# Kernel tuning notes

Measured on AMD Instinct MI355X. Metric: run time of the kernel, lower is better.

## Reference

```python
import jax, jax.numpy as jnp
import numpy as np
import math

MODEL_DIM = 1024
NUM_HEADS = 16
ATTN_DIM = MODEL_DIM // NUM_HEADS  # 64
ROWS, COLS, AXES = 32, 32, 2
PAIRS = ATTN_DIM // (AXES * 2)     # 16
BATCH = 4
TOKENS = ROWS * COLS               # 1024


def setup_inputs() -> dict:
    key = jax.random.key(0)
    ks = jax.random.split(key, 8)
    s = 1.0 / math.sqrt(MODEL_DIM)
    return {
        "x": jax.random.normal(ks[0], (BATCH, TOKENS, MODEL_DIM), jnp.float32),
        "cos": jax.random.uniform(ks[1], (ROWS, COLS, AXES, PAIRS), jnp.float32),
        "sin": jax.random.uniform(ks[2], (ROWS, COLS, AXES, PAIRS), jnp.float32),
        "Wq": jax.random.normal(ks[3], (MODEL_DIM, MODEL_DIM), jnp.float32) * s,
        "Wk": jax.random.normal(ks[4], (MODEL_DIM, MODEL_DIM), jnp.float32) * s,
        "Wv": jax.random.normal(ks[5], (MODEL_DIM, MODEL_DIM), jnp.float32) * s,
        "Wo": jax.random.normal(ks[6], (MODEL_DIM, MODEL_DIM), jnp.float32) * s,
        "bo": jax.random.normal(ks[7], (MODEL_DIM,), jnp.float32) * 0.01,
    }


def _apply_rope(W, cos, sin):
    # W: (b, h, tokens, attn_dim) -> (b, h, rows, cols, axes, pairs, 2)
    b, h, n, d = W.shape
    rows, cols, axes, pairs = cos.shape
    Wp = W.reshape(b, h, rows, cols, axes, pairs, 2)
    c = cos[None, None]
    s = sin[None, None]
    w0, w1 = Wp[..., 0], Wp[..., 1]
    out = jnp.stack([c * w0 - s * w1, s * w0 + c * w1], axis=-1)
    return out.reshape(b, h, n, d)


def reference(x, cos, sin, Wq, Wk, Wv, Wo, bo):
    b, n, _ = x.shape
    # torch Linear: y = x @ W.T
    Q = (x @ Wq.T).reshape(b, n, NUM_HEADS, ATTN_DIM).transpose(0, 2, 1, 3)
    K = (x @ Wk.T).reshape(b, n, NUM_HEADS, ATTN_DIM).transpose(0, 2, 1, 3)
    V = (x @ Wv.T).reshape(b, n, NUM_HEADS, ATTN_DIM).transpose(0, 2, 1, 3)
    Q = _apply_rope(Q, cos, sin)
    K = _apply_rope(K, cos, sin)
    scores = jnp.einsum("bhqd,bhkd->bhqk", Q, K) / math.sqrt(ATTN_DIM)
    attn = jax.nn.softmax(scores, axis=-1)
    o = jnp.einsum("bhqk,bhkd->bhqd", attn, V)
    o = o.transpose(0, 2, 1, 3).reshape(b, n, MODEL_DIM)
    return o @ Wo.T + bo
```

## Files before the change

kernel.cpp:

```cpp
#include <hip/hip_runtime.h>
#include <hip/hip_bf16.h>

typedef __bf16 bf16;
typedef __bf16 bf16x4 __attribute__((ext_vector_type(4)));
typedef __bf16 bf16x8 __attribute__((ext_vector_type(8)));
typedef float  f32x4  __attribute__((ext_vector_type(4)));
typedef unsigned int u32x2 __attribute__((ext_vector_type(2)));

#define MFMA16(a, b, c) __builtin_amdgcn_mfma_f32_16x16x32_bf16((a), (b), (c), 0, 0, 0)

#define GLOBAL_AS(p) ((const __attribute__((address_space(1))) void*)(p))
#define LDS_AS(p)    ((__attribute__((address_space(3))) void*)(p))

#define BATCH 4
#define TOK   1024
#define DIM   1024
#define HEADS 16
#define HD    64
#define MTOT  (BATCH * TOK)
#define MELEM (1024u * 1024u)

__global__ __launch_bounds__(256) void k_prep(
    const float* __restrict__ X,
    const float* __restrict__ W0, const float* __restrict__ W1,
    const float* __restrict__ W2, const float* __restrict__ W3,
    bf16* __restrict__ xh, bf16* __restrict__ wsp)
{
    const int bid = blockIdx.x;
    if (bid < 2048) {
        size_t i0 = ((size_t)bid * 256 + threadIdx.x) * 8;
        f32x4 a = *(const f32x4*)(X + i0);
        f32x4 b = *(const f32x4*)(X + i0 + 4);
        bf16x8 h;
        #pragma unroll
        for (int j = 0; j < 4; j++) { h[j] = (bf16)a[j]; h[4 + j] = (bf16)b[j]; }
        *(bf16x8*)(xh + i0) = h;
    } else {
        const int b2 = bid - 2048;
        const int widx = b2 >> 9;
        const int inner = b2 & 511;
        const float* W = (widx == 0) ? W0 : (widx == 1) ? W1 : (widx == 2) ? W2 : W3;
        size_t i0 = ((size_t)inner * 256 + threadIdx.x) * 8;
        f32x4 a = *(const f32x4*)(W + i0);
        f32x4 b = *(const f32x4*)(W + i0 + 4);
        bf16x8 h, l;
        #pragma unroll
        for (int j = 0; j < 4; j++) {
            bf16 g0 = (bf16)a[j]; h[j] = g0;     l[j] = (bf16)(a[j] - (float)g0);
            bf16 g1 = (bf16)b[j]; h[4 + j] = g1; l[4 + j] = (bf16)(b[j] - (float)g1);
        }
        *(bf16x8*)(wsp + (size_t)widx * MELEM + i0) = h;
        if (widx == 3)
            *(bf16x8*)(wsp + 4 * (size_t)MELEM + i0) = l;
    }
}

__global__ __launch_bounds__(512) void k_gemmQKV(
    const bf16* __restrict__ Ag, const bf16* __restrict__ wsp,
    const float* __restrict__ cosT, const float* __restrict__ sinT,
    bf16* __restrict__ q_o, bf16* __restrict__ k_o, bf16* __restrict__ v_o)
{
    __shared__ bf16 lds[24576];
    bf16* A0 = lds;
    bf16* A1 = lds + 4096;
    bf16* B0 = lds + 8192;
    bf16* B1 = lds + 16384;

    const int fid = blockIdx.x;
    const int swz = (fid & 7) * 48 + (fid >> 3);
    const int nt = swz % 12;
    const int mt = swz / 12;

    const int t = threadIdx.x;
    const int lane = t & 63;
    const int w = t >> 6;
    const int wr = w >> 2, wc = w & 3;
    const int l15 = lane & 15;
    const int grp = lane >> 4;

    f32x4 acc[4][4];
    #pragma unroll
    for (int m = 0; m < 4; m++)
        #pragma unroll
        for (int n = 0; n < 4; n++)
            #pragma unroll
            for (int r = 0; r < 4; r++) acc[m][n][r] = 0.f;

    const int srow = lane >> 2;
    const int schk8 = ((lane & 3) ^ ((lane >> 3) & 3)) * 8;
    const bf16* asrc = Ag  + (size_t)(mt * 128 + srow) * DIM + schk8;
    const bf16* bsrc = wsp + (size_t)(nt * 256 + srow) * DIM + schk8;

    auto stage = [&](int k, bf16* ab, bf16* bb) {
        const int k0 = k * 32;
        __builtin_amdgcn_global_load_lds(
            GLOBAL_AS(asrc + (size_t)w * 16 * DIM + k0),
            LDS_AS(ab + w * 512), 16, 0, 0);
        #pragma unroll
        for (int jj = 0; jj < 2; ++jj) {
            int j = w * 2 + jj;
            __builtin_amdgcn_global_load_lds(
                GLOBAL_AS(bsrc + (size_t)j * 16 * DIM + k0),
                LDS_AS(bb + j * 512), 16, 0, 0);
        }
    };

    auto compute = [&](const bf16* ab, const bf16* bb) {
        bf16x8 fb[4];
        #pragma unroll
        for (int n = 0; n < 4; n++) {
            int rb = wc * 64 + n * 16 + l15;
            fb[n] = *(const bf16x8*)&bb[rb * 32 + ((grp ^ ((rb >> 1) & 3)) << 3)];
        }
        __builtin_amdgcn_s_setprio(1);
        #pragma unroll
        for (int m = 0; m < 4; m++) {
            int r = wr * 64 + m * 16 + l15;
            bf16x8 fa = *(const bf16x8*)&ab[r * 32 + ((grp ^ ((r >> 1) & 3)) << 3)];
            #pragma unroll
            for (int n = 0; n < 4; n++)
                acc[m][n] = MFMA16(fa, fb[n], acc[m][n]);
        }
        __builtin_amdgcn_s_setprio(0);
    };

    stage(0, A0, B0);
    #pragma unroll 1
    for (int kk = 0; kk < 16; kk++) {
        __syncthreads();
        stage(2 * kk + 1, A1, B1);
        compute(A0, B0);
        __syncthreads();
        if (kk < 15) stage(2 * kk + 2, A0, B0);
        compute(A1, B1);
    }

    const int mode = nt >> 2;
    const int h = (nt & 3) * 4 + wc;
    if (mode == 2) {
        #pragma unroll
        for (int m = 0; m < 4; m++) {
            const int grow0 = mt * 128 + wr * 64 + m * 16 + grp * 4;
            const int b = grow0 >> 10, ntok0 = grow0 & (TOK - 1);
            #pragma unroll
            for (int n = 0; n < 4; n++) {
                const int d = n * 16 + l15;
                bf16x4 pk;
                #pragma unroll
                for (int r = 0; r < 4; r++) pk[r] = (bf16)acc[m][n][r];
                *(bf16x4*)&v_o[((size_t)((b * HEADS + h) * HD + d)) * TOK + ntok0] = pk;
            }
        }
    } else {
        __syncthreads();
        float* cosL = (float*)lds;
        float* sinL = (float*)(lds + 8192);
        const int tb = (mt & 7) * 128;
        *(f32x4*)(cosL + t * 8)     = *(const f32x4*)(cosT + (size_t)tb * 32 + t * 8);
        *(f32x4*)(cosL + t * 8 + 4) = *(const f32x4*)(cosT + (size_t)tb * 32 + t * 8 + 4);
        *(f32x4*)(sinL + t * 8)     = *(const f32x4*)(sinT + (size_t)tb * 32 + t * 8);
        *(f32x4*)(sinL + t * 8 + 4) = *(const f32x4*)(sinT + (size_t)tb * 32 + t * 8 + 4);
        __syncthreads();

        bf16* dst = (mode == 0) ? q_o : k_o;
        const float sc = (mode == 0) ? 0.18033688f : 1.0f;
        #pragma unroll
        for (int m = 0; m < 4; m++) {
            const int grow0 = mt * 128 + wr * 64 + m * 16 + grp * 4;
            const int b = grow0 >> 10, ntok0 = grow0 & (TOK - 1);
            const int loc0 = wr * 64 + m * 16 + grp * 4;
            #pragma unroll
            for (int n = 0; n < 4; n++) {
                const int d = n * 16 + l15;
                const int idp = (d >> 5) * 16 + ((d >> 1) & 15);
                const bool ev = (d & 1) == 0;
                #pragma unroll
                for (int r = 0; r < 4; r++) {
                    float v = acc[m][n][r];
                    float pr = __shfl_xor(v, 1, 64);
                    float c = cosL[(loc0 + r) * 32 + idp];
                    float s = sinL[(loc0 + r) * 32 + idp];
                    float res = (ev ? (c * v - s * pr) : (s * pr + c * v)) * sc;
                    dst[((size_t)(b * HEADS + h) * TOK + ntok0 + r) * HD + d] = (bf16)res;
                }
            }
        }
    }
}

__global__ __launch_bounds__(256) void k_gemmO(
    const bf16* __restrict__ Ag, const bf16* __restrict__ wsp,
    const float* __restrict__ bo, float* __restrict__ f_o)
{
    __shared__ bf16 Alin[64 * 64];
    __shared__ bf16 Bhlin[128 * 64];
    __shared__ bf16 Bllin[128 * 64];

    const bf16* Bh_g = wsp + 3 * (size_t)MELEM;
    const bf16* Bl_g = wsp + 4 * (size_t)MELEM;

    const int fid = blockIdx.x;
    const int swz = (fid & 7) * 64 + (fid >> 3);
    const int nt = swz & 7;
    const int mt = swz >> 3;

    const int t = threadIdx.x;
    const int lane = t & 63;
    const int w = t >> 6;
    const int wr = w >> 1, wc = w & 1;
    const int l15 = lane & 15;

    f32x4 acc[2][4];
    #pragma unroll
    for (int m = 0; m < 2; m++)
        #pragma unroll
        for (int n = 0; n < 4; n++)
            #pragma unroll
            for (int r = 0; r < 4; r++) acc[m][n][r] = 0.f;

    const int srow = lane >> 3;
    const int schk8 = ((lane & 7) ^ (srow & 7)) * 8;
    const bf16* asrc  = Ag   + (size_t)(mt * 64 + srow) * DIM + schk8;
    const bf16* bhsrc = Bh_g + (size_t)(nt * 128 + srow) * DIM + schk8;
    const bf16* blsrc = Bl_g + (size_t)(nt * 128 + srow) * DIM + schk8;

    for (int k0 = 0; k0 < DIM; k0 += 64) {
        __syncthreads();
        #pragma unroll
        for (int ii = 0; ii < 2; ++ii) {
            int i = w * 2 + ii;
            __builtin_amdgcn_global_load_lds(
                GLOBAL_AS(asrc + (size_t)i * 8 * DIM + k0),
                LDS_AS(&Alin[i * 512]), 16, 0, 0);
        }
        #pragma unroll
        for (int jj = 0; jj < 4; ++jj) {
            int j = w * 4 + jj;
            size_t roff = (size_t)j * 8 * DIM + k0;
            __builtin_amdgcn_global_load_lds(GLOBAL_AS(bhsrc + roff),
                                             LDS_AS(&Bhlin[j * 512]), 16, 0, 0);
            __builtin_amdgcn_global_load_lds(GLOBAL_AS(blsrc + roff),
                                             LDS_AS(&Bllin[j * 512]), 16, 0, 0);
        }
        __syncthreads();

        #pragma unroll
        for (int ks = 0; ks < 2; ks++) {
            const int cc = (lane >> 4) + ks * 4;
            bf16x8 fbh[4], fbl[4];
            #pragma unroll
            for (int n = 0; n < 4; n++) {
                int r = wc * 64 + n * 16 + l15;
                int off = r * 64 + ((cc ^ (r & 7)) << 3);
                fbh[n] = *(const bf16x8*)&Bhlin[off];
                fbl[n] = *(const bf16x8*)&Bllin[off];
            }
            #pragma unroll
            for (int m = 0; m < 2; m++) {
                int r = wr * 32 + m * 16 + l15;
                bf16x8 fa = *(const bf16x8*)&Alin[r * 64 + ((cc ^ (r & 7)) << 3)];
                #pragma unroll
                for (int n = 0; n < 4; n++) {
                    acc[m][n] = MFMA16(fa, fbh[n], acc[m][n]);
                    acc[m][n] = MFMA16(fa, fbl[n], acc[m][n]);
                }
            }
        }
    }

    #pragma unroll
    for (int m = 0; m < 2; m++) {
        #pragma unroll
        for (int n = 0; n < 4; n++) {
            const int grow0 = mt * 64 + wr * 32 + m * 16 + (lane >> 4) * 4;
            const int gcol  = nt * 128 + wc * 64 + n * 16 + l15;
            const float bias = bo[gcol];
            #pragma unroll
            for (int r = 0; r < 4; r++)
                f_o[(size_t)(grow0 + r) * DIM + gcol] = acc[m][n][r] + bias;
        }
    }
}

__global__ __launch_bounds__(256) void k_attn(
    const bf16* __restrict__ Q, const bf16* __restrict__ K,
    const bf16* __restrict__ Vt, bf16* __restrict__ O)
{
    __shared__ bf16 Ks0[64 * 64];
    __shared__ bf16 Ks1[64 * 64];
    __shared__ bf16 Vs0[64 * 64];
    __shared__ bf16 Vs1[64 * 64];
    __shared__ bf16 Ps[64 * 64];

    const int fid = blockIdx.x;
    const int swz = (fid & 7) * 128 + (fid >> 3);
    const int qt = swz & 15;
    const int bh = swz >> 4;

    const int t = threadIdx.x;
    const int lane = t & 63;
    const int w = t >> 6;
    const int col = lane & 15;
    const int grp = lane >> 4;
    const int m7 = col & 7;
    const int qrow = w * 16 + col;

    const bf16* qp = Q + ((size_t)bh * TOK + qt * 64 + qrow) * HD + grp * 8;
    bf16x8 qf0 = *(const bf16x8*)qp;
    bf16x8 qf1 = *(const bf16x8*)(qp + 32);

    const int srow = lane >> 3;
    const int schk8 = ((lane & 7) ^ (srow & 7)) * 8;
    const bf16* ksrc = K  + ((size_t)bh * TOK + srow) * HD + schk8;
    const bf16* vsrc = Vt + ((size_t)bh * HD + srow) * TOK + schk8;

    bf16x8 ones;
    #pragma unroll
    for (int j = 0; j < 8; j++) ones[j] = (bf16)1.0f;

    f32x4 zero = {0.f, 0.f, 0.f, 0.f};
    f32x4 lacc = zero;
    f32x4 o_[4];
    #pragma unroll
    for (int dt = 0; dt < 4; dt++) o_[dt] = zero;

    unsigned int* PsU = (unsigned int*)Ps;

    auto stageK = [&](int kt, bf16* kb) {
        #pragma unroll
        for (int ii = 0; ii < 2; ++ii) {
            int i = w * 2 + ii;
            __builtin_amdgcn_global_load_lds(
                GLOBAL_AS(ksrc + (size_t)(kt * 64 + i * 8) * HD),
                LDS_AS(kb + i * 512), 16, 0, 0);
        }
    };
    auto stageV = [&](int kt, bf16* vb) {
        #pragma unroll
        for (int ii = 0; ii < 2; ++ii) {
            int i = w * 2 + ii;
            __builtin_amdgcn_global_load_lds(
                GLOBAL_AS(vsrc + (size_t)(i * 8) * TOK + kt * 64),
                LDS_AS(vb + i * 512), 16, 0, 0);
        }
    };

    auto qkt = [&](const bf16* kb, f32x4* s) {
        #pragma unroll
        for (int ct = 0; ct < 4; ct++) s[ct] = zero;
        __builtin_amdgcn_s_setprio(1);
        #pragma unroll
        for (int ct = 0; ct < 4; ct++) {
            int rbase = (ct * 16 + col) * 64;
            bf16x8 kf0 = *(const bf16x8*)&kb[rbase + ((grp ^ m7) << 3)];
            bf16x8 kf1 = *(const bf16x8*)&kb[rbase + (((grp + 4) ^ m7) << 3)];
            s[ct] = MFMA16(kf0, qf0, s[ct]);
            s[ct] = MFMA16(kf1, qf1, s[ct]);
        }
        __builtin_amdgcn_s_setprio(0);
    };

    auto packpv = [&](const f32x4* s, const bf16* vb) {
        #pragma unroll
        for (int ct = 0; ct < 4; ct++) {
            float p0 = exp2f(s[ct][0]);
            float p1 = exp2f(s[ct][1]);
            float p2 = exp2f(s[ct][2]);
            float p3 = exp2f(s[ct][3]);
            unsigned int a0, a1;
            asm("v_cvt_pk_bf16_f32 %0, %1, %2" : "=v"(a0) : "v"(p0), "v"(p1));
            asm("v_cvt_pk_bf16_f32 %0, %1, %2" : "=v"(a1) : "v"(p2), "v"(p3));
            int cs = (2 * ct + (grp >> 1)) ^ m7;
            u32x2 st = {a0, a1};
            *(u32x2*)&PsU[qrow * 32 + cs * 4 + (grp & 1) * 2] = st;
        }
        __builtin_amdgcn_s_setprio(1);
        #pragma unroll
        for (int tt = 0; tt < 2; tt++) {
            const int coff = ((4 * tt + grp) ^ m7) << 3;
            bf16x8 pf = *(const bf16x8*)&Ps[qrow * 64 + coff];
            lacc = MFMA16(ones, pf, lacc);
            #pragma unroll
            for (int dt = 0; dt < 4; dt++) {
                bf16x8 vf = *(const bf16x8*)&vb[(dt * 16 + col) * 64 + coff];
                o_[dt] = MFMA16(vf, pf, o_[dt]);
            }
        }
        __builtin_amdgcn_s_setprio(0);
    };

    f32x4 sa[4], sprev[4];

    stageK(0, Ks0);
    stageV(0, Vs0);
    #pragma unroll 1
    for (int kk = 0; kk < 8; kk++) {
        __syncthreads();
        stageK(2 * kk + 1, Ks1);
        if (kk > 0) stageV(2 * kk, Vs0);
        qkt(Ks0, sa);
        if (kk > 0) packpv(sprev, Vs1);
        __syncthreads();
        if (kk < 7) stageK(2 * kk + 2, Ks0);
        stageV(2 * kk + 1, Vs1);
        qkt(Ks1, sprev);
        packpv(sa, Vs0);
    }
    __syncthreads();
    packpv(sprev, Vs1);

    const float inv = 1.0f / lacc[0];

    const int b = bh >> 4, h = bh & 15;
    const int ntok = qt * 64 + qrow;
    #pragma unroll
    for (int dt = 0; dt < 4; dt++) {
        bf16x4 pk4;
        #pragma unroll
        for (int r = 0; r < 4; r++) pk4[r] = (bf16)(o_[dt][r] * inv);
        *(bf16x4*)&O[((size_t)b * TOK + ntok) * DIM + h * HD + dt * 16 + grp * 4] = pk4;
    }
}

extern "C" void kernel_launch(void* const* d_in, const int* in_sizes, int n_in,
                              void* d_out, int out_size, void* d_ws, size_t ws_size,
                              hipStream_t stream)
{
    const float* x    = (const float*)d_in[0];
    const float* cosT = (const float*)d_in[1];
    const float* sinT = (const float*)d_in[2];
    const float* Wq   = (const float*)d_in[3];
    const float* Wk   = (const float*)d_in[4];
    const float* Wv   = (const float*)d_in[5];
    const float* Wo   = (const float*)d_in[6];
    const float* bo   = (const float*)d_in[7];
    float* out = (float*)d_out;

    bf16* xh  = (bf16*)d_ws;
    bf16* qw  = xh + 4 * (size_t)MELEM;
    bf16* kw  = qw + 4 * (size_t)MELEM;
    bf16* vw  = kw + 4 * (size_t)MELEM;
    bf16* wsp = vw + 4 * (size_t)MELEM;
    bf16* ow  = xh;

    k_prep<<<dim3(4096), dim3(256), 0, stream>>>(x, Wq, Wk, Wv, Wo, xh, wsp);
    k_gemmQKV<<<dim3(384), dim3(512), 0, stream>>>(xh, wsp, cosT, sinT, qw, kw, vw);
    k_attn<<<dim3(1024), dim3(256), 0, stream>>>(qw, kw, vw, ow);
    k_gemmO<<<dim3(512), dim3(256), 0, stream>>>(ow, wsp, bo, out);
}
```

Measured before the change: 98.92 us.

## Fuse fp32-to-bf16 conversion of x and QKV weights into the QKV GEMM

Removes the separate prep pass that converted x and Wq/Wk/Wv to bf16. The QKV GEMM now loads fp32 tiles into registers, converts them and writes them to swizzled LDS, with register prefetch replacing the async global-to-LDS loads. A small kernel still splits Wo into hi/lo bf16 parts. This saves the round trip of writing and re-reading bf16 copies, but the GEMM reads twice the bytes per tile and the new synchronous staging can overlap less with compute.

```diff
diff --git a/kernel.cpp b/kernel.cpp
--- a/kernel.cpp
+++ b/kernel.cpp
@@ -20,43 +20,25 @@
 #define MTOT  (BATCH * TOK)
 #define MELEM (1024u * 1024u)
 
-__global__ __launch_bounds__(256) void k_prep(
+__global__ __launch_bounds__(256) void k_prepO(
+    const float* __restrict__ Wo, bf16* __restrict__ wsp)
+{
+    size_t i0 = ((size_t)blockIdx.x * 256 + threadIdx.x) * 8;
+    f32x4 a = *(const f32x4*)(Wo + i0);
+    f32x4 b = *(const f32x4*)(Wo + i0 + 4);
+    bf16x8 h, l;
+    #pragma unroll
+    for (int j = 0; j < 4; j++) {
+        bf16 g0 = (bf16)a[j]; h[j] = g0;     l[j] = (bf16)(a[j] - (float)g0);
+        bf16 g1 = (bf16)b[j]; h[4 + j] = g1; l[4 + j] = (bf16)(b[j] - (float)g1);
+    }
+    *(bf16x8*)(wsp + i0) = h;
+    *(bf16x8*)(wsp + (size_t)MELEM + i0) = l;
+}
+
+__global__ __launch_bounds__(512) void k_gemmQKV(
     const float* __restrict__ X,
-    const float* __restrict__ W0, const float* __restrict__ W1,
-    const float* __restrict__ W2, const float* __restrict__ W3,
-    bf16* __restrict__ xh, bf16* __restrict__ wsp)
-{
-    const int bid = blockIdx.x;
-    if (bid < 2048) {
-        size_t i0 = ((size_t)bid * 256 + threadIdx.x) * 8;
-        f32x4 a = *(const f32x4*)(X + i0);
-        f32x4 b = *(const f32x4*)(X + i0 + 4);
-        bf16x8 h;
-        #pragma unroll
-        for (int j = 0; j < 4; j++) { h[j] = (bf16)a[j]; h[4 + j] = (bf16)b[j]; }
-        *(bf16x8*)(xh + i0) = h;
-    } else {
-        const int b2 = bid - 2048;
-        const int widx = b2 >> 9;
-        const int inner = b2 & 511;
-        const float* W = (widx == 0) ? W0 : (widx == 1) ? W1 : (widx == 2) ? W2 : W3;
-        size_t i0 = ((size_t)inner * 256 + threadIdx.x) * 8;
-        f32x4 a = *(const f32x4*)(W + i0);
-        f32x4 b = *(const f32x4*)(W + i0 + 4);
-        bf16x8 h, l;
-        #pragma unroll
-        for (int j = 0; j < 4; j++) {
-            bf16 g0 = (bf16)a[j]; h[j] = g0;     l[j] = (bf16)(a[j] - (float)g0);
-            bf16 g1 = (bf16)b[j]; h[4 + j] = g1; l[4 + j] = (bf16)(b[j] - (float)g1);
-        }
-        *(bf16x8*)(wsp + (size_t)widx * MELEM + i0) = h;
-        if (widx == 3)
-            *(bf16x8*)(wsp + 4 * (size_t)MELEM + i0) = l;
-    }
-}
-
-__global__ __launch_bounds__(512) void k_gemmQKV(
-    const bf16* __restrict__ Ag, const bf16* __restrict__ wsp,
+    const float* __restrict__ Wq, const float* __restrict__ Wk, const float* __restrict__ Wv,
     const float* __restrict__ cosT, const float* __restrict__ sinT,
     bf16* __restrict__ q_o, bf16* __restrict__ k_o, bf16* __restrict__ v_o)
 {
@@ -78,6 +60,9 @@
     const int l15 = lane & 15;
     const int grp = lane >> 4;
 
+    const int mode = nt >> 2;
+    const float* Wsel = (mode == 0) ? Wq : (mode == 1) ? Wk : Wv;
+
     f32x4 acc[4][4];
     #pragma unroll
     for (int m = 0; m < 4; m++)
@@ -86,23 +71,37 @@
             #pragma unroll
             for (int r = 0; r < 4; r++) acc[m][n][r] = 0.f;
 
-    const int srow = lane >> 2;
-    const int schk8 = ((lane & 3) ^ ((lane >> 3) & 3)) * 8;
-    const bf16* asrc = Ag  + (size_t)(mt * 128 + srow) * DIM + schk8;
-    const bf16* bsrc = wsp + (size_t)(nt * 256 + srow) * DIM + schk8;
-
-    auto stage = [&](int k, bf16* ab, bf16* bb) {
-        const int k0 = k * 32;
-        __builtin_amdgcn_global_load_lds(
-            GLOBAL_AS(asrc + (size_t)w * 16 * DIM + k0),
-            LDS_AS(ab + w * 512), 16, 0, 0);
-        #pragma unroll
-        for (int jj = 0; jj < 2; ++jj) {
-            int j = w * 2 + jj;
-            __builtin_amdgcn_global_load_lds(
-                GLOBAL_AS(bsrc + (size_t)j * 16 * DIM + k0),
-                LDS_AS(bb + j * 512), 16, 0, 0);
-        }
+    const int arow = t >> 2, acg = t & 3;
+    const float* aF = X + (size_t)(mt * 128 + arow) * DIM + acg * 8;
+    const int aoff = arow * 32 + ((acg ^ ((arow >> 1) & 3)) << 3);
+    const int brow = t >> 1, bhf = t & 1;
+    const float* bF = Wsel + (size_t)((nt & 3) * 256 + brow) * DIM + bhf * 16;
+    const int bc0 = bhf * 2;
+    const int boff0 = brow * 32 + ((bc0 ^ ((brow >> 1) & 3)) << 3);
+    const int boff1 = brow * 32 + (((bc0 + 1) ^ ((brow >> 1) & 3)) << 3);
+
+    f32x4 ra0, ra1, rb0, rb1, rb2, rb3;
+    auto loadregs = [&](int k) {
+        const float* ap = aF + k * 32;
+        ra0 = *(const f32x4*)ap;
+        ra1 = *(const f32x4*)(ap + 4);
+        const float* bp = bF + k * 32;
+        rb0 = *(const f32x4*)bp;
+        rb1 = *(const f32x4*)(bp + 4);
+        rb2 = *(const f32x4*)(bp + 8);
+        rb3 = *(const f32x4*)(bp + 12);
+    };
+    auto cvtwrite = [&](bf16* ab, bf16* bb) {
+        bf16x8 va, vb0, vb1;
+        #pragma unroll
+        for (int j = 0; j < 4; j++) {
+            va[j] = (bf16)ra0[j];  va[4 + j] = (bf16)ra1[j];
+            vb0[j] = (bf16)rb0[j]; vb0[4 + j] = (bf16)rb1[j];
+            vb1[j] = (bf16)rb2[j]; vb1[4 + j] = (bf16)rb3[j];
+        }
+        *(bf16x8*)&ab[aoff]  = va;
+        *(bf16x8*)&bb[boff0] = vb0;
+        *(bf16x8*)&bb[boff1] = vb1;
     };
 
     auto compute = [&](const bf16* ab, const bf16* bb) {
@@ -124,18 +123,21 @@
         __builtin_amdgcn_s_setprio(0);
     };
 
-    stage(0, A0, B0);
+    loadregs(0);
+    cvtwrite(A0, B0);
+    __syncthreads();
     #pragma unroll 1
     for (int kk = 0; kk < 16; kk++) {
-        __syncthreads();
-        stage(2 * kk + 1, A1, B1);
+        loadregs(2 * kk + 1);
         compute(A0, B0);
-        __syncthreads();
-        if (kk < 15) stage(2 * kk + 2, A0, B0);
+        cvtwrite(A1, B1);
+        __syncthreads();
+        if (kk < 15) loadregs(2 * kk + 2);
         compute(A1, B1);
-    }
-
-    const int mode = nt >> 2;
+        if (kk < 15) cvtwrite(A0, B0);
+        __syncthreads();
+    }
+
     const int h = (nt & 3) * 4 + wc;
     if (mode == 2) {
         #pragma unroll
@@ -196,8 +198,8 @@
     __shared__ bf16 Bhlin[128 * 64];
     __shared__ bf16 Bllin[128 * 64];
 
-    const bf16* Bh_g = wsp + 3 * (size_t)MELEM;
-    const bf16* Bl_g = wsp + 4 * (size_t)MELEM;
+    const bf16* Bh_g = wsp;
+    const bf16* Bl_g = wsp + (size_t)MELEM;
 
     const int fid = blockIdx.x;
     const int swz = (fid & 7) * 64 + (fid >> 3);
@@ -436,15 +438,14 @@
     const float* bo   = (const float*)d_in[7];
     float* out = (float*)d_out;
 
-    bf16* xh  = (bf16*)d_ws;
-    bf16* qw  = xh + 4 * (size_t)MELEM;
+    bf16* ow  = (bf16*)d_ws;
+    bf16* qw  = ow + 4 * (size_t)MELEM;
     bf16* kw  = qw + 4 * (size_t)MELEM;
     bf16* vw  = kw + 4 * (size_t)MELEM;
     bf16* wsp = vw + 4 * (size_t)MELEM;
-    bf16* ow  = xh;
-
-    k_prep<<<dim3(4096), dim3(256), 0, stream>>>(x, Wq, Wk, Wv, Wo, xh, wsp);
-    k_gemmQKV<<<dim3(384), dim3(512), 0, stream>>>(xh, wsp, cosT, sinT, qw, kw, vw);
+
+    k_prepO<<<dim3(512), dim3(256), 0, stream>>>(Wo, wsp);
+    k_gemmQKV<<<dim3(384), dim3(512), 0, stream>>>(x, Wq, Wk, Wv, cosT, sinT, qw, kw, vw);
     k_attn<<<dim3(1024), dim3(256), 0, stream>>>(qw, kw, vw, ow);
     k_gemmO<<<dim3(512), dim3(256), 0, stream>>>(ow, wsp, bo, out);
 }
```

After: 135.5 us. 36.9% more time.
